# Kernel tuning notes

Measured on AMD Instinct MI355X. Metric: run time of the kernel, lower is better.

## Reference

```python
import jax, jax.numpy as jnp
import numpy as np

K = 5
TOPK_WEIGHT = 3.0
B, N = 4096, 4096


def setup_inputs() -> dict:
    key = jax.random.key(0)
    k1, k2 = jax.random.split(key)
    preds = jax.random.normal(k1, (B, N), dtype=jnp.float32)
    targets = jax.random.normal(k2, (B, N), dtype=jnp.float32)
    return {"preds": preds, "targets": targets}


def reference(preds, targets):
    # per-row squared error
    loss = (preds - targets) ** 2  # [B, N]
    b, n = targets.shape
    k = min(K, n)
    # batched top-k over last dim (indices only; values unused)
    _, top_idx = jax.lax.top_k(targets, k)  # [B, k]
    rows = jnp.arange(b)[:, None]  # [B, 1]
    weights = jnp.ones_like(targets).at[rows, top_idx].set(TOPK_WEIGHT)
    return (loss * weights).mean()
```

## Files before the change

### kernel.cpp

```cpp
#include <hip/hip_runtime.h>
#include <stdint.h>


static constexpr int BDIM = 512;
static constexpr int NROW = 4096;
static constexpr int NCOL = 4096;
static constexpr int NWAVE = BDIM / 64;

__device__ __forceinline__ uint32_t f32_mono(float f) {
    uint32_t u = __float_as_uint(f);
    return u ^ (uint32_t)(((int32_t)u >> 31) | (int32_t)0x80000000);
}

__device__ __forceinline__ uint32_t umaxu(uint32_t a, uint32_t b) { return a > b ? a : b; }

__global__ __launch_bounds__(BDIM) void wmse_rows(const float* __restrict__ preds,
                                                  const float* __restrict__ tgts,
                                                  float* __restrict__ rowsum) {
    const int row = blockIdx.x;
    const int tid = threadIdx.x;
    const int lane = tid & 63;
    const int wave = tid >> 6;

    const float4* p4 = reinterpret_cast<const float4*>(preds) + (size_t)row * (NCOL / 4);
    const float4* t4 = reinterpret_cast<const float4*>(tgts) + (size_t)row * (NCOL / 4);

    const float4 pa = p4[tid];
    const float4 pb = p4[tid + BDIM];
    const float4 ta = t4[tid];
    const float4 tb = t4[tid + BDIM];

    float loss[8];
    uint32_t key[8];
    {
        const float d0 = pa.x - ta.x, d1 = pa.y - ta.y, d2 = pa.z - ta.z, d3 = pa.w - ta.w;
        const float e0 = pb.x - tb.x, e1 = pb.y - tb.y, e2 = pb.z - tb.z, e3 = pb.w - tb.w;
        loss[0] = d0 * d0; loss[1] = d1 * d1; loss[2] = d2 * d2; loss[3] = d3 * d3;
        loss[4] = e0 * e0; loss[5] = e1 * e1; loss[6] = e2 * e2; loss[7] = e3 * e3;
        key[0] = f32_mono(ta.x); key[1] = f32_mono(ta.y); key[2] = f32_mono(ta.z); key[3] = f32_mono(ta.w);
        key[4] = f32_mono(tb.x); key[5] = f32_mono(tb.y); key[6] = f32_mono(tb.z); key[7] = f32_mono(tb.w);
    }
    float ssq = ((loss[0] + loss[1]) + (loss[2] + loss[3])) +
                ((loss[4] + loss[5]) + (loss[6] + loss[7]));

    __shared__ uint32_t cand[NWAVE * 5];
    __shared__ uint32_t s_tau;
    __shared__ float fred[NWAVE];

    {
        uint32_t prev = 0xFFFFFFFFu;
#pragma unroll
        for (int r = 0; r < 5; ++r) {
            uint32_t c = 0u;
#pragma unroll
            for (int i = 0; i < 8; ++i) {
                c = (key[i] < prev) ? umaxu(c, key[i]) : c;
            }
#pragma unroll
            for (int sh = 32; sh >= 1; sh >>= 1) {
                uint32_t o = (uint32_t)__shfl_xor((int)c, sh, 64);
                c = umaxu(c, o);
            }
            if (lane == 0) cand[wave * 5 + r] = c;
            prev = c;
        }
    }
    __syncthreads();

    if (wave == 0) {
        uint32_t c0 = (lane < NWAVE * 5) ? cand[lane] : 0u;
        uint32_t prev = 0xFFFFFFFFu;
#pragma unroll
        for (int r = 0; r < 5; ++r) {
            uint32_t c = (c0 < prev) ? c0 : 0u;
#pragma unroll
            for (int sh = 32; sh >= 1; sh >>= 1) {
                uint32_t o = (uint32_t)__shfl_xor((int)c, sh, 64);
                c = umaxu(c, o);
            }
            prev = c;
        }
        if (lane == 0) s_tau = prev;
    }
    __syncthreads();
    const uint32_t tau = s_tau;

    float extra = 0.f;
#pragma unroll
    for (int i = 0; i < 8; ++i) {
        extra += (key[i] >= tau) ? loss[i] : 0.f;
    }

    float part = ssq + 2.0f * extra;
#pragma unroll
    for (int sh = 32; sh >= 1; sh >>= 1) {
        part += __shfl_xor(part, sh, 64);
    }
    if (lane == 0) fred[wave] = part;
    __syncthreads();
    if (tid == 0) {
        float tot = 0.f;
#pragma unroll
        for (int w = 0; w < NWAVE; ++w) tot += fred[w];
        rowsum[row] = tot;
    }
}

__global__ __launch_bounds__(256) void wmse_reduce(const float* __restrict__ rowsum,
                                                   float* __restrict__ out) {
    double acc = 0.0;
    for (int i = threadIdx.x; i < NROW; i += 256) {
        acc += (double)rowsum[i];
    }
#pragma unroll
    for (int sh = 32; sh >= 1; sh >>= 1) {
        acc += __shfl_xor(acc, sh, 64);
    }
    __shared__ double dred[4];
    if ((threadIdx.x & 63) == 0) dred[threadIdx.x >> 6] = acc;
    __syncthreads();
    if (threadIdx.x == 0) {
        const double tot = dred[0] + dred[1] + dred[2] + dred[3];
        out[0] = (float)(tot / ((double)NROW * (double)NCOL));
    }
}

extern "C" void kernel_launch(void* const* d_in, const int* in_sizes, int n_in,
                              void* d_out, int out_size, void* d_ws, size_t ws_size,
                              hipStream_t stream) {
    const float* preds = (const float*)d_in[0];
    const float* tgts = (const float*)d_in[1];
    float* rowsum = (float*)d_ws;
    float* out = (float*)d_out;

    wmse_rows<<<NROW, BDIM, 0, stream>>>(preds, tgts, rowsum);
    wmse_reduce<<<1, 256, 0, stream>>>(rowsum, out);
}
```

Baseline: 32.52 us.

## Split rows into wave-sized chunks with per-chunk top-5 and separate merge kernel

Each wave now handles one 512-element chunk of a row by itself and computes that chunk's top-5, packing each target key with its loss into a 64-bit value, so no block-level barriers or LDS are needed. A second kernel gives one row per thread, merges the 40 candidates by insertion into a top-5 and adds the row's chunk sums. A third kernel finishes the reduction. This removes the __syncthreads and the cross-wave shuffles of the per-row block, at the cost of two extra launches and workspace traffic for the candidates. Tie handling changes from threshold comparison to exact packed ordering.

```diff
diff --git a/kernel.cpp b/kernel.cpp
--- a/kernel.cpp
+++ b/kernel.cpp
@@ -2,126 +2,123 @@
 #include <stdint.h>
 
 
-static constexpr int BDIM = 512;
+typedef unsigned long long u64;
+
 static constexpr int NROW = 4096;
 static constexpr int NCOL = 4096;
-static constexpr int NWAVE = BDIM / 64;
+static constexpr int CHUNK = 512;
+static constexpr int CPR = NCOL / CHUNK;
+static constexpr int NCHUNK = NROW * CPR;
+static constexpr int WPB = 4;
+static constexpr int BDIM = WPB * 64;
 
 __device__ __forceinline__ uint32_t f32_mono(float f) {
     uint32_t u = __float_as_uint(f);
     return u ^ (uint32_t)(((int32_t)u >> 31) | (int32_t)0x80000000);
 }
 
-__device__ __forceinline__ uint32_t umaxu(uint32_t a, uint32_t b) { return a > b ? a : b; }
+__global__ __launch_bounds__(BDIM) void wmse_chunks(const float* __restrict__ preds,
+                                                    const float* __restrict__ tgts,
+                                                    u64* __restrict__ top5,
+                                                    float* __restrict__ ssqs) {
+    const int chunk = blockIdx.x * WPB + (threadIdx.x >> 6);
+    const int lane = threadIdx.x & 63;
 
-__global__ __launch_bounds__(BDIM) void wmse_rows(const float* __restrict__ preds,
-                                                  const float* __restrict__ tgts,
-                                                  float* __restrict__ rowsum) {
-    const int row = blockIdx.x;
-    const int tid = threadIdx.x;
-    const int lane = tid & 63;
-    const int wave = tid >> 6;
+    const float4* p4 = reinterpret_cast<const float4*>(preds) + (size_t)chunk * (CHUNK / 4) + lane;
+    const float4* t4 = reinterpret_cast<const float4*>(tgts) + (size_t)chunk * (CHUNK / 4) + lane;
 
-    const float4* p4 = reinterpret_cast<const float4*>(preds) + (size_t)row * (NCOL / 4);
-    const float4* t4 = reinterpret_cast<const float4*>(tgts) + (size_t)row * (NCOL / 4);
+    const float4 pa = p4[0];
+    const float4 pb = p4[64];
+    const float4 ta = t4[0];
+    const float4 tb = t4[64];
 
-    const float4 pa = p4[tid];
-    const float4 pb = p4[tid + BDIM];
-    const float4 ta = t4[tid];
-    const float4 tb = t4[tid + BDIM];
-
-    float loss[8];
-    uint32_t key[8];
+    float ls[8];
+    u64 pk[8];
     {
         const float d0 = pa.x - ta.x, d1 = pa.y - ta.y, d2 = pa.z - ta.z, d3 = pa.w - ta.w;
         const float e0 = pb.x - tb.x, e1 = pb.y - tb.y, e2 = pb.z - tb.z, e3 = pb.w - tb.w;
-        loss[0] = d0 * d0; loss[1] = d1 * d1; loss[2] = d2 * d2; loss[3] = d3 * d3;
-        loss[4] = e0 * e0; loss[5] = e1 * e1; loss[6] = e2 * e2; loss[7] = e3 * e3;
-        key[0] = f32_mono(ta.x); key[1] = f32_mono(ta.y); key[2] = f32_mono(ta.z); key[3] = f32_mono(ta.w);
-        key[4] = f32_mono(tb.x); key[5] = f32_mono(tb.y); key[6] = f32_mono(tb.z); key[7] = f32_mono(tb.w);
-    }
-    float ssq = ((loss[0] + loss[1]) + (loss[2] + loss[3])) +
-                ((loss[4] + loss[5]) + (loss[6] + loss[7]));
-
-    __shared__ uint32_t cand[NWAVE * 5];
-    __shared__ uint32_t s_tau;
-    __shared__ float fred[NWAVE];
-
-    {
-        uint32_t prev = 0xFFFFFFFFu;
-#pragma unroll
-        for (int r = 0; r < 5; ++r) {
-            uint32_t c = 0u;
-#pragma unroll
-            for (int i = 0; i < 8; ++i) {
-                c = (key[i] < prev) ? umaxu(c, key[i]) : c;
-            }
-#pragma unroll
-            for (int sh = 32; sh >= 1; sh >>= 1) {
-                uint32_t o = (uint32_t)__shfl_xor((int)c, sh, 64);
-                c = umaxu(c, o);
-            }
-            if (lane == 0) cand[wave * 5 + r] = c;
-            prev = c;
-        }
-    }
-    __syncthreads();
-
-    if (wave == 0) {
-        uint32_t c0 = (lane < NWAVE * 5) ? cand[lane] : 0u;
-        uint32_t prev = 0xFFFFFFFFu;
-#pragma unroll
-        for (int r = 0; r < 5; ++r) {
-            uint32_t c = (c0 < prev) ? c0 : 0u;
-#pragma unroll
-            for (int sh = 32; sh >= 1; sh >>= 1) {
-                uint32_t o = (uint32_t)__shfl_xor((int)c, sh, 64);
-                c = umaxu(c, o);
-            }
-            prev = c;
-        }
-        if (lane == 0) s_tau = prev;
-    }
-    __syncthreads();
-    const uint32_t tau = s_tau;
-
-    float extra = 0.f;
-#pragma unroll
-    for (int i = 0; i < 8; ++i) {
-        extra += (key[i] >= tau) ? loss[i] : 0.f;
+        ls[0] = d0 * d0; ls[1] = d1 * d1; ls[2] = d2 * d2; ls[3] = d3 * d3;
+        ls[4] = e0 * e0; ls[5] = e1 * e1; ls[6] = e2 * e2; ls[7] = e3 * e3;
+        pk[0] = ((u64)f32_mono(ta.x) << 32) | __float_as_uint(ls[0]);
+        pk[1] = ((u64)f32_mono(ta.y) << 32) | __float_as_uint(ls[1]);
+        pk[2] = ((u64)f32_mono(ta.z) << 32) | __float_as_uint(ls[2]);
+        pk[3] = ((u64)f32_mono(ta.w) << 32) | __float_as_uint(ls[3]);
+        pk[4] = ((u64)f32_mono(tb.x) << 32) | __float_as_uint(ls[4]);
+        pk[5] = ((u64)f32_mono(tb.y) << 32) | __float_as_uint(ls[5]);
+        pk[6] = ((u64)f32_mono(tb.z) << 32) | __float_as_uint(ls[6]);
+        pk[7] = ((u64)f32_mono(tb.w) << 32) | __float_as_uint(ls[7]);
     }
 
-    float part = ssq + 2.0f * extra;
+    float ssq = ((ls[0] + ls[1]) + (ls[2] + ls[3])) + ((ls[4] + ls[5]) + (ls[6] + ls[7]));
 #pragma unroll
     for (int sh = 32; sh >= 1; sh >>= 1) {
-        part += __shfl_xor(part, sh, 64);
+        ssq += __shfl_xor(ssq, sh, 64);
     }
-    if (lane == 0) fred[wave] = part;
-    __syncthreads();
-    if (tid == 0) {
-        float tot = 0.f;
+
+    u64 prev = ~0ull;
+    u64 mine = 0;
 #pragma unroll
-        for (int w = 0; w < NWAVE; ++w) tot += fred[w];
-        rowsum[row] = tot;
+    for (int r = 0; r < 5; ++r) {
+        u64 c = 0;
+#pragma unroll
+        for (int i = 0; i < 8; ++i) {
+            c = (pk[i] < prev && pk[i] > c) ? pk[i] : c;
+        }
+#pragma unroll
+        for (int sh = 32; sh >= 1; sh >>= 1) {
+            const u64 o = __shfl_xor(c, sh, 64);
+            c = (o > c) ? o : c;
+        }
+        if (lane == r) mine = c;
+        prev = c;
     }
+
+    if (lane < 5) top5[(size_t)chunk * 5 + lane] = mine;
+    if (lane == 0) ssqs[chunk] = ssq;
 }
 
-__global__ __launch_bounds__(256) void wmse_reduce(const float* __restrict__ rowsum,
-                                                   float* __restrict__ out) {
-    double acc = 0.0;
-    for (int i = threadIdx.x; i < NROW; i += 256) {
-        acc += (double)rowsum[i];
+__global__ __launch_bounds__(64) void wmse_merge(const u64* __restrict__ top5,
+                                                 const float* __restrict__ ssqs,
+                                                 double* __restrict__ partials) {
+    const int row = blockIdx.x * 64 + threadIdx.x;
+    const u64* t = top5 + (size_t)row * (5 * CPR);
+
+    u64 s0 = 0, s1 = 0, s2 = 0, s3 = 0, s4 = 0;
+#pragma unroll
+    for (int j = 0; j < 5 * CPR; ++j) {
+        u64 v = t[j], m;
+        m = s0 > v ? s0 : v; v = s0 > v ? v : s0; s0 = m;
+        m = s1 > v ? s1 : v; v = s1 > v ? v : s1; s1 = m;
+        m = s2 > v ? s2 : v; v = s2 > v ? v : s2; s2 = m;
+        m = s3 > v ? s3 : v; v = s3 > v ? v : s3; s3 = m;
+        m = s4 > v ? s4 : v; v = s4 > v ? v : s4; s4 = m;
     }
+    const float extra = __uint_as_float((uint32_t)s0) + __uint_as_float((uint32_t)s1) +
+                        __uint_as_float((uint32_t)s2) + __uint_as_float((uint32_t)s3) +
+                        __uint_as_float((uint32_t)s4);
+    float ss = 0.f;
+#pragma unroll
+    for (int q = 0; q < CPR; ++q) {
+        ss += ssqs[row * CPR + q];
+    }
+
+    double rsum = (double)ss + 2.0 * (double)extra;
 #pragma unroll
     for (int sh = 32; sh >= 1; sh >>= 1) {
-        acc += __shfl_xor(acc, sh, 64);
+        rsum += __shfl_xor(rsum, sh, 64);
     }
-    __shared__ double dred[4];
-    if ((threadIdx.x & 63) == 0) dred[threadIdx.x >> 6] = acc;
-    __syncthreads();
+    if (threadIdx.x == 0) partials[blockIdx.x] = rsum;
+}
+
+__global__ __launch_bounds__(64) void wmse_final(const double* __restrict__ partials,
+                                                 float* __restrict__ out) {
+    double v = partials[threadIdx.x];
+#pragma unroll
+    for (int sh = 32; sh >= 1; sh >>= 1) {
+        v += __shfl_xor(v, sh, 64);
+    }
     if (threadIdx.x == 0) {
-        const double tot = dred[0] + dred[1] + dred[2] + dred[3];
-        out[0] = (float)(tot / ((double)NROW * (double)NCOL));
+        out[0] = (float)(v / ((double)NROW * (double)NCOL));
     }
 }
 
@@ -130,9 +127,13 @@
                               hipStream_t stream) {
     const float* preds = (const float*)d_in[0];
     const float* tgts = (const float*)d_in[1];
-    float* rowsum = (float*)d_ws;
+
+    u64* top5 = (u64*)d_ws;
+    float* ssqs = (float*)((char*)d_ws + 1310720);
+    double* partials = (double*)((char*)d_ws + 1441792);
     float* out = (float*)d_out;
 
-    wmse_rows<<<NROW, BDIM, 0, stream>>>(preds, tgts, rowsum);
-    wmse_reduce<<<1, 256, 0, stream>>>(rowsum, out);
+    wmse_chunks<<<NCHUNK / WPB, BDIM, 0, stream>>>(preds, tgts, top5, ssqs);
+    wmse_merge<<<NROW / 64, 64, 0, stream>>>(top5, ssqs, partials);
+    wmse_final<<<1, 64, 0, stream>>>(partials, out);
 }
```

Measured after the change: 39.49 us. +21.4%, slower.
